# Performance work log

Hardware: AMD Instinct MI355X
Metric: run time of the kernel (lower is better)

## Reference

```python
import jax, jax.numpy as jnp
import numpy as np

N = 128          # cube side (voxels)
LPIX = 3.0       # Mpc per voxel (hardcoded in dsq_loss.forward)
KBINS = 100      # radial k bins (hardcoded)
LOSS_WEIGHT = 1.0


def _binning(n, lpix, kbins):
    # Static radial k-bin assignment computed once with numpy.
    kf = 2.0 * np.pi * np.fft.fftfreq(n, d=lpix)
    kx, ky, kz = np.meshgrid(kf, kf, kf, indexing='ij')
    kmag = np.sqrt(kx * kx + ky * ky + kz * kz).ravel()  # [n^3]
    pos = kmag > 0
    edges = np.linspace(kmag[pos].min(), kmag.max(), kbins + 1)
    ids = np.clip(np.digitize(kmag, edges) - 1, 0, kbins - 1)
    ids = np.where(pos, ids, kbins)  # route k=0 (DC) mode to a dropped bin
    counts = np.bincount(ids[pos], minlength=kbins).astype(np.float32)
    kcent = 0.5 * (edges[:-1] + edges[1:])
    return ids.astype(np.int32), counts, kcent.astype(np.float32)

_IDS, _COUNTS, _KCENT = _binning(N, LPIX, KBINS)


def _dsq(x):
    # x: [B, 1, N, N, N] -> dimensionless power spectrum Delta^2(k): [B, KBINS]
    b = x.shape[0]
    fk = jnp.fft.fftn(x, axes=(-3, -2, -1))
    # P(k) estimator: |delta_k|^2 * Lpix^3 / N^3  (Lpix^6/V with V=(N*Lpix)^3)
    pk = (fk.real ** 2 + fk.imag ** 2) * (LPIX ** 3 / float(N ** 3))
    pk = pk.reshape(b, -1).T  # [N^3, B]
    sums = jax.ops.segment_sum(pk, jnp.asarray(_IDS), num_segments=KBINS + 1)[:KBINS]
    cnt = jnp.asarray(_COUNTS)[:, None]
    pmean = jnp.where(cnt > 0, sums / jnp.maximum(cnt, 1.0), jnp.nan)  # [KBINS, B]
    kc = jnp.asarray(_KCENT)[:, None]
    dsq = pmean * kc ** 3 / (2.0 * jnp.pi ** 2)
    return dsq.T  # [B, KBINS]


def setup_inputs() -> dict:
    key = jax.random.key(0)
    k1, k2 = jax.random.split(key)
    # positive brightness-temperature-like fields so log10(Delta^2) is finite
    pred = jax.random.uniform(k1, (8, 1, N, N, N), dtype=jnp.float32) + 0.1
    target = jax.random.uniform(k2, (8, 1, N, N, N), dtype=jnp.float32) + 0.1
    return {"pred": pred, "target": target}


def reference(pred, target):
    dsq_hr = _dsq(target)
    dsq_sr = _dsq(pred)
    loss = jnp.nanmean(jnp.abs(jnp.log10(dsq_hr) - jnp.log10(dsq_sr)))
    return LOSS_WEIGHT * loss
```

## Files before the change

kernel.cpp:

```cpp
#include <hip/hip_runtime.h>
#include <math.h>

#ifndef M_PI
#define M_PI 3.14159265358979323846
#endif

#define NSIDE 128
#define NVOX  2097152
#define KBINS 100
#define NFIELDS 16
#define NORMF (27.0f / 2097152.0f)
#define FSTRIDE ((size_t)65 * 16384)


#define WS_SUMS_OFF   0
#define WS_CNT_OFF    6464
#define WS_OCT_OFF    8192
#define WS_TRANS_OFF  282880

__device__ __forceinline__ double bin_edge(int i, double start, double step, double stop) {
    if (i == 100) return stop;
    return __dadd_rn(__dmul_rn((double)i, step), start);
}

__device__ __forceinline__ void bin_params(double* start, double* step, double* stop) {
    const double inv   = 1.0 / 384.0;
    const double twopi = 2.0 * M_PI;
    double k1 = __dmul_rn(twopi, __dmul_rn(1.0, inv));
    *start = sqrt(__dadd_rn(__dadd_rn(0.0, 0.0), __dmul_rn(k1, k1)));
    double k64 = __dmul_rn(twopi, __dmul_rn(-64.0, inv));
    double s64 = __dmul_rn(k64, k64);
    *stop = sqrt(__dadd_rn(__dadd_rn(s64, s64), s64));
    *step = (*stop - *start) / 100.0;
}

__device__ int compute_bin(int ix, int iy, int iz) {
    const double inv   = 1.0 / 384.0;
    const double twopi = 2.0 * M_PI;
    double fx = (double)(ix < 64 ? ix : ix - 128);
    double fy = (double)(iy < 64 ? iy : iy - 128);
    double fz = (double)(iz < 64 ? iz : iz - 128);
    double kx = __dmul_rn(twopi, __dmul_rn(fx, inv));
    double ky = __dmul_rn(twopi, __dmul_rn(fy, inv));
    double kz = __dmul_rn(twopi, __dmul_rn(fz, inv));
    double sq = __dadd_rn(__dadd_rn(__dmul_rn(kx, kx), __dmul_rn(ky, ky)), __dmul_rn(kz, kz));
    double kmag = sqrt(sq);
    if (!(kmag > 0.0)) return 100;
    double start, step, stop;
    bin_params(&start, &step, &stop);
    double t = (kmag - start) / step;
    int c = (int)floor(t);
    if (c < -1) c = -1;
    if (c > 100) c = 100;
    while (c < 100 && kmag >= bin_edge(c + 1, start, step, stop)) ++c;
    while (c >= 0 && kmag < bin_edge(c, start, step, stop)) --c;
    if (c < 0) c = 0;
    if (c > 99) c = 99;
    return c;
}

__device__ __forceinline__ int br3(int v) { return ((v & 1) << 2) | (v & 2) | ((v >> 2) & 1); }
__device__ __forceinline__ int br4(int v) {
    return ((v & 1) << 3) | ((v & 2) << 1) | ((v & 4) >> 1) | ((v & 8) >> 3);
}

__device__ __forceinline__ float2 f2add(float2 a, float2 b) { return make_float2(a.x + b.x, a.y + b.y); }
__device__ __forceinline__ float2 f2sub(float2 a, float2 b) { return make_float2(a.x - b.x, a.y - b.y); }
__device__ __forceinline__ float2 cmul(float2 a, float2 w) {
    return make_float2(a.x * w.x - a.y * w.y, a.x * w.y + a.y * w.x);
}
__device__ __forceinline__ float2 twid(float r) {
    return make_float2(__builtin_amdgcn_cosf(r), __builtin_amdgcn_sinf(r));
}

__device__ __forceinline__ void fft128_r16(float2 r[16], int m) {
    const float fm = (float)m;
#pragma unroll
    for (int j = 0; j < 8; ++j) {
        float2 W = twid(-(fm + 8.0f * (float)j) * (1.0f / 128.0f));
        float2 a = r[j], b = r[j + 8];
        r[j]     = f2add(a, b);
        r[j + 8] = cmul(f2sub(a, b), W);
    }
#pragma unroll
    for (int j = 0; j < 4; ++j) {
        float2 W = twid(-(fm + 8.0f * (float)j) * (1.0f / 64.0f));
#pragma unroll
        for (int half = 0; half < 16; half += 8) {
            float2 a = r[half + j], b = r[half + j + 4];
            r[half + j]     = f2add(a, b);
            r[half + j + 4] = cmul(f2sub(a, b), W);
        }
    }
#pragma unroll
    for (int j = 0; j < 2; ++j) {
        float2 W = twid(-(fm + 8.0f * (float)j) * (1.0f / 32.0f));
#pragma unroll
        for (int q = 0; q < 16; q += 4) {
            float2 a = r[q + j], b = r[q + j + 2];
            r[q + j]     = f2add(a, b);
            r[q + j + 2] = cmul(f2sub(a, b), W);
        }
    }
    {
        float2 W = twid(-fm * (1.0f / 16.0f));
#pragma unroll
        for (int q = 0; q < 16; q += 2) {
            float2 a = r[q], b = r[q + 1];
            r[q]     = f2add(a, b);
            r[q + 1] = cmul(f2sub(a, b), W);
        }
    }
#pragma unroll
    for (int h = 4; h >= 2; h >>= 1) {
        bool hi = (m & h) != 0;
        float2 W = twid(-(float)(m & (h - 1)) / (float)(2 * h));
#pragma unroll
        for (int j = 0; j < 16; ++j) {
            float2 x = r[j];
            float2 v = make_float2(__shfl_xor(x.x, h, 64), __shfl_xor(x.y, h, 64));
            float2 s = f2add(x, v);
            float2 d = cmul(f2sub(v, x), W);
            r[j] = hi ? d : s;
        }
    }
    {
        bool hi = (m & 1) != 0;
#pragma unroll
        for (int j = 0; j < 16; ++j) {
            float2 x = r[j];
            float2 v = make_float2(__shfl_xor(x.x, 1, 64), __shfl_xor(x.y, 1, 64));
            r[j] = hi ? f2sub(v, x) : f2add(x, v);
        }
    }
}

__device__ __forceinline__ void fft128_c16(float2 r[16], int m) {
    const float S2 = 0.70710678118654752f;
    {
        int q = m & 3;
        float2 Wm = make_float2(q == 0 ? 1.f : (q == 1 ? S2 : (q == 2 ? 0.f : -S2)),
                                q == 0 ? 0.f : (q == 2 ? -1.f : -S2));
        bool hi = (m & 4) != 0;
        const float2 C[16] = {
            {1.f,0.f},{0.99879546f,-0.04906767f},{0.99518473f,-0.09801714f},
            {0.98917651f,-0.14673047f},{0.98078528f,-0.19509032f},{0.97003125f,-0.24298018f},
            {0.95694034f,-0.29028468f},{0.94154407f,-0.33688985f},{0.92387953f,-0.38268343f},
            {0.90398929f,-0.42755509f},{0.88192126f,-0.47139674f},{0.85772861f,-0.51410274f},
            {0.83146961f,-0.55557023f},{0.80320753f,-0.59569930f},{0.77301045f,-0.63439328f},
            {0.74095113f,-0.67155895f} };
#pragma unroll
        for (int j = 0; j < 16; ++j) {
            float2 x = r[j];
            float2 v = make_float2(__shfl_xor(x.x, 4, 64), __shfl_xor(x.y, 4, 64));
            float2 s = f2add(x, v);
            float2 d = cmul(cmul(f2sub(v, x), Wm), C[j]);
            r[j] = hi ? d : s;
        }
    }
    {
        bool w = (m & 1) != 0;
        bool hi = (m & 2) != 0;
        const float2 C[16] = {
            {1.f,0.f},{0.99518473f,-0.09801714f},{0.98078528f,-0.19509032f},
            {0.95694034f,-0.29028468f},{0.92387953f,-0.38268343f},{0.88192126f,-0.47139674f},
            {0.83146961f,-0.55557023f},{0.77301045f,-0.63439328f},{S2,-S2},
            {0.63439328f,-0.77301045f},{0.55557023f,-0.83146961f},{0.47139674f,-0.88192126f},
            {0.38268343f,-0.92387953f},{0.29028468f,-0.95694034f},{0.19509032f,-0.98078528f},
            {0.09801714f,-0.99518473f} };
#pragma unroll
        for (int j = 0; j < 16; ++j) {
            float2 x = r[j];
            float2 v = make_float2(__shfl_xor(x.x, 2, 64), __shfl_xor(x.y, 2, 64));
            float2 s = f2add(x, v);
            float2 d = f2sub(v, x);
            d = w ? make_float2(d.y, -d.x) : d;
            d = cmul(d, C[j]);
            r[j] = hi ? d : s;
        }
    }
    {
        bool hi = (m & 1) != 0;
        const float2 C[16] = {
            {1.f,0.f},{0.98078528f,-0.19509032f},{0.92387953f,-0.38268343f},
            {0.83146961f,-0.55557023f},{S2,-S2},{0.55557023f,-0.83146961f},
            {0.38268343f,-0.92387953f},{0.19509032f,-0.98078528f},{0.f,-1.f},
            {-0.19509032f,-0.98078528f},{-0.38268343f,-0.92387953f},{-0.55557023f,-0.83146961f},
            {-S2,-S2},{-0.83146961f,-0.55557023f},{-0.92387953f,-0.38268343f},
            {-0.98078528f,-0.19509032f} };
#pragma unroll
        for (int j = 0; j < 16; ++j) {
            float2 x = r[j];
            float2 v = make_float2(__shfl_xor(x.x, 1, 64), __shfl_xor(x.y, 1, 64));
            float2 s = f2add(x, v);
            float2 d = cmul(f2sub(v, x), C[j]);
            r[j] = hi ? d : s;
        }
    }
    {
        const float2 C[8] = {
            {1.f,0.f},{0.92387953f,-0.38268343f},{S2,-S2},{0.38268343f,-0.92387953f},
            {0.f,-1.f},{-0.38268343f,-0.92387953f},{-S2,-S2},{-0.92387953f,-0.38268343f} };
#pragma unroll
        for (int j = 0; j < 8; ++j) {
            float2 a = r[j], b = r[j + 8];
            r[j]     = f2add(a, b);
            r[j + 8] = cmul(f2sub(a, b), C[j]);
        }
    }
    {
        const float2 C[4] = { {1.f,0.f},{S2,-S2},{0.f,-1.f},{-S2,-S2} };
#pragma unroll
        for (int q = 0; q < 16; q += 8)
#pragma unroll
            for (int j = 0; j < 4; ++j) {
                float2 a = r[q + j], b = r[q + j + 4];
                r[q + j]     = f2add(a, b);
                r[q + j + 4] = cmul(f2sub(a, b), C[j]);
            }
    }
    {
#pragma unroll
        for (int q = 0; q < 16; q += 4) {
            { float2 a = r[q], b = r[q + 2]; r[q] = f2add(a, b); r[q + 2] = f2sub(a, b); }
            { float2 a = r[q + 1], b = r[q + 3]; float2 d = f2sub(a, b);
              r[q + 1] = f2add(a, b); r[q + 3] = make_float2(d.y, -d.x); }
        }
    }
    {
#pragma unroll
        for (int q = 0; q < 16; q += 2) {
            float2 a = r[q], b = r[q + 1];
            r[q] = f2add(a, b); r[q + 1] = f2sub(a, b);
        }
    }
}

__global__ __launch_bounds__(256) void k_zero(float* sums, int* counts) {
    int t = blockIdx.x * 256 + threadIdx.x;
    if (t < NFIELDS * 101) sums[t] = 0.0f;
    if (t < 101) counts[t] = 0;
}

__global__ __launch_bounds__(256) void k_oct(unsigned char* __restrict__ oct,
                                             int* __restrict__ counts) {
    __shared__ int lcnt[4][104];
    int tid = threadIdx.x;
#pragma unroll
    for (int j = tid; j < 4 * 104; j += 256) ((int*)lcnt)[j] = 0;
    __syncthreads();
    int idx = blockIdx.x * 256 + tid;
    if (idx < 65 * 65 * 65) {
        int c = idx % 65;
        int r = idx / 65;
        int b = r % 65;
        int a = r / 65;
        int id = compute_bin(a, b, c);
        oct[c * 4225 + a * 65 + b] = (unsigned char)id;
        if (id < 100) {
            int w = ((a == 0 || a == 64) ? 1 : 2) *
                    ((b == 0 || b == 64) ? 1 : 2) *
                    ((c == 0 || c == 64) ? 1 : 2);
            atomicAdd(&lcnt[tid & 3][id], w);
        }
    }
    __syncthreads();
    if (tid < 101) {
        int tot = lcnt[0][tid] + lcnt[1][tid] + lcnt[2][tid] + lcnt[3][tid];
        if (tot) atomicAdd(&counts[tid], tot);
    }
}

__global__ __launch_bounds__(512, 4) void k_fft_zy(const float* __restrict__ pred,
                                                   const float* __restrict__ target,
                                                   float2* __restrict__ A) {
    __shared__ float2 lds[65][132];
    int t = threadIdx.x;
    int m = t & 7, row = t >> 3;
    int x = blockIdx.x;
    int f = blockIdx.y;
    const float* in = (f < 8) ? (pred + (size_t)f * NVOX)
                              : (target + (size_t)(f - 8) * NVOX);

    int b3 = br3(m);
#pragma unroll
    for (int y0 = 0; y0 < 128; y0 += 64) {
        int y = y0 + row;
        const float4* s4 = reinterpret_cast<const float4*>(
            in + (size_t)x * 16384 + (size_t)y * 128 + 16 * m);
        float2 r[16];
#pragma unroll
        for (int q = 0; q < 4; ++q) {
            float4 v = s4[q];
            r[4 * q + 0] = make_float2(v.x, 0.f);
            r[4 * q + 1] = make_float2(v.y, 0.f);
            r[4 * q + 2] = make_float2(v.z, 0.f);
            r[4 * q + 3] = make_float2(v.w, 0.f);
        }
        fft128_c16(r, m);
#pragma unroll
        for (int j = 0; j < 16; j += 2) {
            int kz = 8 * br4(j) + b3;
            lds[kz][y] = r[j];
        }
        if (m == 0) lds[64][y] = r[1];
    }
    __syncthreads();

    float2* basef = A + (size_t)f * FSTRIDE + (size_t)x * 8;
#pragma unroll
    for (int k0 = 0; k0 < 128; k0 += 64) {
        int kz = k0 + row;
        if (kz <= 64) {
            float2 r[16];
#pragma unroll
            for (int j = 0; j < 16; ++j) r[j] = lds[kz][m + 8 * j];
            fft128_r16(r, m);
            float2* dst = basef + (size_t)kz * 16384;
#pragma unroll
            for (int j = 0; j < 16; ++j) dst[j * 1024 + m] = r[j];
        }
    }
}

__global__ __launch_bounds__(256, 6) void k_fft_x_bin(const float2* __restrict__ A,
                                                      const unsigned char* __restrict__ oct,
                                                      float* __restrict__ sums) {
    __shared__ __align__(16) float lbins[8][104];
    __shared__ __align__(16) unsigned char ltab[4384];
    int t = threadIdx.x;
    int m = t & 7, g = t >> 3;
    int kz = blockIdx.x >> 2;
    int s0 = (blockIdx.x & 3) << 5;
    int f = blockIdx.y;
    int p = s0 + g;

    const float2* base = A + (size_t)f * FSTRIDE + (size_t)kz * 16384
                           + (size_t)(p >> 3) * 1024 + (p & 7);
    float2 r[16];
#pragma unroll
    for (int j = 0; j < 16; ++j) r[j] = base[8 * m + 64 * j];

    if (t < 208) ((float4*)lbins)[t] = make_float4(0.f, 0.f, 0.f, 0.f);
    int rowb = kz * 4225;
    int ab   = rowb & ~15;
    int pad  = rowb & 15;
    const uint4* osrc = (const uint4*)(oct + ab);
    ((uint4*)ltab)[t] = osrc[t];
    if (t < 14) ((uint4*)ltab)[256 + t] = osrc[256 + t];

    asm volatile("" : "+v"(r[0]), "+v"(r[1]), "+v"(r[2]), "+v"(r[3]),
                      "+v"(r[4]), "+v"(r[5]), "+v"(r[6]), "+v"(r[7]),
                      "+v"(r[8]), "+v"(r[9]), "+v"(r[10]), "+v"(r[11]),
                      "+v"(r[12]), "+v"(r[13]), "+v"(r[14]), "+v"(r[15]));
    fft128_r16(r, m);
    __syncthreads();

    const unsigned char* lt = ltab + pad;
    int ky = (br3(p & 7) << 4) | br4(p >> 3);
    int mky = (ky <= 64) ? ky : 128 - ky;
    int b3x = br3(m) << 4;
#pragma unroll
    for (int j = 0; j < 16; ++j) {
        int kx = b3x | br4(j);
        int mkx = (kx <= 64) ? kx : 128 - kx;
        float pk = r[j].x * r[j].x + r[j].y * r[j].y;
        atomicAdd(&lbins[t & 7][lt[mkx * 65 + mky]], pk);
    }
    __syncthreads();
    if (t < 101) {
        float wz = (kz == 0 || kz == 64) ? 1.0f : 2.0f;
        float v = lbins[0][t] + lbins[1][t] + lbins[2][t] + lbins[3][t] +
                  lbins[4][t] + lbins[5][t] + lbins[6][t] + lbins[7][t];
        if (v != 0.0f) atomicAdd(&sums[f * 101 + t], v * (NORMF) * wz);
    }
}

__global__ __launch_bounds__(128) void k_finalize(const float* __restrict__ sums,
                                                  const int* __restrict__ counts,
                                                  float* __restrict__ out) {
    __shared__ double ssum[128];
    __shared__ int scnt[128];
    int k = threadIdx.x;
    double local = 0.0;
    int nloc = 0;
    if (k < KBINS) {
        int c = counts[k];
        if (c > 0) {
            double start, step, stop;
            bin_params(&start, &step, &stop);
            double e0 = bin_edge(k, start, step, stop);
            double e1 = bin_edge(k + 1, start, step, stop);
            float kc  = (float)(0.5 * (e0 + e1));
            float kc3 = kc * kc * kc;
            const float two_pi2 = (float)(2.0 * M_PI * M_PI);
            float cf = (float)c;
            for (int b = 0; b < 8; ++b) {
                float pm_p = sums[b * 101 + k] / cf;
                float pm_t = sums[(8 + b) * 101 + k] / cf;
                float dsq_p = pm_p * kc3 / two_pi2;
                float dsq_t = pm_t * kc3 / two_pi2;
                float d = fabsf(log10f(dsq_t) - log10f(dsq_p));
                local += (double)d;
            }
            nloc = 8;
        }
    }
    ssum[k] = local;
    scnt[k] = nloc;
    __syncthreads();
    for (int off = 64; off > 0; off >>= 1) {
        if (k < off) { ssum[k] += ssum[k + off]; scnt[k] += scnt[k + off]; }
        __syncthreads();
    }
    if (k == 0) out[0] = (float)(ssum[0] / (double)scnt[0]);
}

extern "C" void kernel_launch(void* const* d_in, const int* in_sizes, int n_in,
                              void* d_out, int out_size, void* d_ws, size_t ws_size,
                              hipStream_t stream) {
    (void)in_sizes; (void)n_in; (void)out_size; (void)ws_size;
    const float* pred   = (const float*)d_in[0];
    const float* target = (const float*)d_in[1];
    float* out = (float*)d_out;
    char* ws = (char*)d_ws;

    float* sums        = (float*)(ws + WS_SUMS_OFF);
    int* counts        = (int*)(ws + WS_CNT_OFF);
    unsigned char* oct = (unsigned char*)(ws + WS_OCT_OFF);
    float2* A          = (float2*)(ws + WS_TRANS_OFF);

    k_zero<<<7, 256, 0, stream>>>(sums, counts);
    k_oct<<<(65 * 65 * 65 + 255) / 256, 256, 0, stream>>>(oct, counts);

    k_fft_zy<<<dim3(128, NFIELDS), 512, 0, stream>>>(pred, target, A);
    k_fft_x_bin<<<dim3(65 * 4, NFIELDS), 256, 0, stream>>>(A, oct, sums);

    k_finalize<<<1, 128, 0, stream>>>(sums, counts, out);
}
```

Measured before the change: 322.0 us.

## Fuse finalize into x-FFT binning kernel and run-length merge bin atomics

Removes the separate finalize launch: the last block of the x-FFT/binning kernel, found with a global atomic counter, computes the loss. Bin lookups now read the octant table straight from global memory instead of staging it in LDS. Consecutive modes that fall in the same bin are accumulated in registers before one LDS atomic, which cuts atomic traffic. The z-y kernel's kz loop is restructured so only row 0 handles the Nyquist plane, and occupancy hints change from 6 to 4 blocks, which adds tail-block serialisation and extra global byte loads in exchange.

```diff
diff --git a/kernel.cpp b/kernel.cpp
--- a/kernel.cpp
+++ b/kernel.cpp
@@ -11,10 +11,12 @@
 #define NFIELDS 16
 #define NORMF (27.0f / 2097152.0f)
 #define FSTRIDE ((size_t)65 * 16384)
+#define NBLK_XBIN (65 * 4 * NFIELDS)
 
 
 #define WS_SUMS_OFF   0
 #define WS_CNT_OFF    6464
+#define WS_CTR_OFF    7936
 #define WS_OCT_OFF    8192
 #define WS_TRANS_OFF  282880
 
@@ -236,10 +238,11 @@
     }
 }
 
-__global__ __launch_bounds__(256) void k_zero(float* sums, int* counts) {
+__global__ __launch_bounds__(256) void k_zero(float* sums, int* counts, int* ctr) {
     int t = blockIdx.x * 256 + threadIdx.x;
     if (t < NFIELDS * 101) sums[t] = 0.0f;
     if (t < 101) counts[t] = 0;
+    if (t == 101) *ctr = 0;
 }
 
 __global__ __launch_bounds__(256) void k_oct(unsigned char* __restrict__ oct,
@@ -308,26 +311,37 @@
     __syncthreads();
 
     float2* basef = A + (size_t)f * FSTRIDE + (size_t)x * 8;
-#pragma unroll
-    for (int k0 = 0; k0 < 128; k0 += 64) {
-        int kz = k0 + row;
-        if (kz <= 64) {
-            float2 r[16];
-#pragma unroll
-            for (int j = 0; j < 16; ++j) r[j] = lds[kz][m + 8 * j];
-            fft128_r16(r, m);
-            float2* dst = basef + (size_t)kz * 16384;
-#pragma unroll
-            for (int j = 0; j < 16; ++j) dst[j * 1024 + m] = r[j];
-        }
-    }
-}
-
-__global__ __launch_bounds__(256, 6) void k_fft_x_bin(const float2* __restrict__ A,
+    {
+        int kz = row;
+        float2 r[16];
+#pragma unroll
+        for (int j = 0; j < 16; ++j) r[j] = lds[kz][m + 8 * j];
+        fft128_r16(r, m);
+        float2* dst = basef + (size_t)kz * 16384;
+#pragma unroll
+        for (int j = 0; j < 16; ++j) dst[j * 1024 + m] = r[j];
+    }
+    if (row == 0) {
+        float2 r[16];
+#pragma unroll
+        for (int j = 0; j < 16; ++j) r[j] = lds[64][m + 8 * j];
+        fft128_r16(r, m);
+        float2* dst = basef + (size_t)64 * 16384;
+#pragma unroll
+        for (int j = 0; j < 16; ++j) dst[j * 1024 + m] = r[j];
+    }
+}
+
+__global__ __launch_bounds__(256, 4) void k_fft_x_bin(const float2* __restrict__ A,
                                                       const unsigned char* __restrict__ oct,
-                                                      float* __restrict__ sums) {
+                                                      float* __restrict__ sums,
+                                                      const int* __restrict__ counts,
+                                                      int* __restrict__ ctr,
+                                                      float* __restrict__ out) {
     __shared__ __align__(16) float lbins[8][104];
-    __shared__ __align__(16) unsigned char ltab[4384];
+    __shared__ double ssum[256];
+    __shared__ int scnt[256];
+    __shared__ int lastFlag;
     int t = threadIdx.x;
     int m = t & 7, g = t >> 3;
     int kz = blockIdx.x >> 2;
@@ -335,69 +349,80 @@
     int f = blockIdx.y;
     int p = s0 + g;
 
+    if (t < 208) ((float4*)lbins)[t] = make_float4(0.f, 0.f, 0.f, 0.f);
+    __syncthreads();
+
     const float2* base = A + (size_t)f * FSTRIDE + (size_t)kz * 16384
                            + (size_t)(p >> 3) * 1024 + (p & 7);
     float2 r[16];
 #pragma unroll
     for (int j = 0; j < 16; ++j) r[j] = base[8 * m + 64 * j];
-
-    if (t < 208) ((float4*)lbins)[t] = make_float4(0.f, 0.f, 0.f, 0.f);
-    int rowb = kz * 4225;
-    int ab   = rowb & ~15;
-    int pad  = rowb & 15;
-    const uint4* osrc = (const uint4*)(oct + ab);
-    ((uint4*)ltab)[t] = osrc[t];
-    if (t < 14) ((uint4*)ltab)[256 + t] = osrc[256 + t];
-
-    asm volatile("" : "+v"(r[0]), "+v"(r[1]), "+v"(r[2]), "+v"(r[3]),
-                      "+v"(r[4]), "+v"(r[5]), "+v"(r[6]), "+v"(r[7]),
-                      "+v"(r[8]), "+v"(r[9]), "+v"(r[10]), "+v"(r[11]),
-                      "+v"(r[12]), "+v"(r[13]), "+v"(r[14]), "+v"(r[15]));
     fft128_r16(r, m);
-    __syncthreads();
-
-    const unsigned char* lt = ltab + pad;
+
     int ky = (br3(p & 7) << 4) | br4(p >> 3);
     int mky = (ky <= 64) ? ky : 128 - ky;
     int b3x = br3(m) << 4;
-#pragma unroll
-    for (int j = 0; j < 16; ++j) {
-        int kx = b3x | br4(j);
+    const unsigned char* lt = oct + kz * 4225;
+    int bs[16];
+#pragma unroll
+    for (int jj = 0; jj < 16; ++jj) {
+        int kx = b3x + jj;
         int mkx = (kx <= 64) ? kx : 128 - kx;
-        float pk = r[j].x * r[j].x + r[j].y * r[j].y;
-        atomicAdd(&lbins[t & 7][lt[mkx * 65 + mky]], pk);
-    }
-    __syncthreads();
+        bs[jj] = lt[mkx * 65 + mky];
+    }
+
+    {
+        float2 v0 = r[br4(0)];
+        float acc = v0.x * v0.x + v0.y * v0.y;
+        int cur = bs[0];
+#pragma unroll
+        for (int jj = 1; jj < 16; ++jj) {
+            float2 v = r[br4(jj)];
+            float pk = v.x * v.x + v.y * v.y;
+            if (bs[jj] == cur) {
+                acc += pk;
+            } else {
+                atomicAdd(&lbins[m][cur], acc);
+                cur = bs[jj];
+                acc = pk;
+            }
+        }
+        atomicAdd(&lbins[m][cur], acc);
+    }
+    __syncthreads();
+
     if (t < 101) {
         float wz = (kz == 0 || kz == 64) ? 1.0f : 2.0f;
         float v = lbins[0][t] + lbins[1][t] + lbins[2][t] + lbins[3][t] +
                   lbins[4][t] + lbins[5][t] + lbins[6][t] + lbins[7][t];
         if (v != 0.0f) atomicAdd(&sums[f * 101 + t], v * (NORMF) * wz);
     }
-}
-
-__global__ __launch_bounds__(128) void k_finalize(const float* __restrict__ sums,
-                                                  const int* __restrict__ counts,
-                                                  float* __restrict__ out) {
-    __shared__ double ssum[128];
-    __shared__ int scnt[128];
-    int k = threadIdx.x;
+
+    __threadfence();
+    if (t == 0) lastFlag = (atomicAdd(ctr, 1) == NBLK_XBIN - 1);
+    __syncthreads();
+    if (!lastFlag) return;
+
     double local = 0.0;
     int nloc = 0;
-    if (k < KBINS) {
-        int c = counts[k];
+    if (t < KBINS) {
+        int c = __hip_atomic_load(&counts[t], __ATOMIC_RELAXED, __HIP_MEMORY_SCOPE_AGENT);
         if (c > 0) {
             double start, step, stop;
             bin_params(&start, &step, &stop);
-            double e0 = bin_edge(k, start, step, stop);
-            double e1 = bin_edge(k + 1, start, step, stop);
+            double e0 = bin_edge(t, start, step, stop);
+            double e1 = bin_edge(t + 1, start, step, stop);
             float kc  = (float)(0.5 * (e0 + e1));
             float kc3 = kc * kc * kc;
             const float two_pi2 = (float)(2.0 * M_PI * M_PI);
             float cf = (float)c;
             for (int b = 0; b < 8; ++b) {
-                float pm_p = sums[b * 101 + k] / cf;
-                float pm_t = sums[(8 + b) * 101 + k] / cf;
+                float sp = __hip_atomic_load(&sums[b * 101 + t], __ATOMIC_RELAXED,
+                                             __HIP_MEMORY_SCOPE_AGENT);
+                float st = __hip_atomic_load(&sums[(8 + b) * 101 + t], __ATOMIC_RELAXED,
+                                             __HIP_MEMORY_SCOPE_AGENT);
+            float pm_p = sp / cf;
+                float pm_t = st / cf;
                 float dsq_p = pm_p * kc3 / two_pi2;
                 float dsq_t = pm_t * kc3 / two_pi2;
                 float d = fabsf(log10f(dsq_t) - log10f(dsq_p));
@@ -406,14 +431,14 @@
             nloc = 8;
         }
     }
-    ssum[k] = local;
-    scnt[k] = nloc;
-    __syncthreads();
-    for (int off = 64; off > 0; off >>= 1) {
-        if (k < off) { ssum[k] += ssum[k + off]; scnt[k] += scnt[k + off]; }
+    ssum[t] = local;
+    scnt[t] = nloc;
+    __syncthreads();
+    for (int off = 128; off > 0; off >>= 1) {
+        if (t < off) { ssum[t] += ssum[t + off]; scnt[t] += scnt[t + off]; }
         __syncthreads();
     }
-    if (k == 0) out[0] = (float)(ssum[0] / (double)scnt[0]);
+    if (t == 0) out[0] = (float)(ssum[0] / (double)scnt[0]);
 }
 
 extern "C" void kernel_launch(void* const* d_in, const int* in_sizes, int n_in,
@@ -427,14 +452,13 @@
 
     float* sums        = (float*)(ws + WS_SUMS_OFF);
     int* counts        = (int*)(ws + WS_CNT_OFF);
+    int* ctr           = (int*)(ws + WS_CTR_OFF);
     unsigned char* oct = (unsigned char*)(ws + WS_OCT_OFF);
     float2* A          = (float2*)(ws + WS_TRANS_OFF);
 
-    k_zero<<<7, 256, 0, stream>>>(sums, counts);
+    k_zero<<<7, 256, 0, stream>>>(sums, counts, ctr);
     k_oct<<<(65 * 65 * 65 + 255) / 256, 256, 0, stream>>>(oct, counts);
 
     k_fft_zy<<<dim3(128, NFIELDS), 512, 0, stream>>>(pred, target, A);
-    k_fft_x_bin<<<dim3(65 * 4, NFIELDS), 256, 0, stream>>>(A, oct, sums);
-
-    k_finalize<<<1, 128, 0, stream>>>(sums, counts, out);
-}
+    k_fft_x_bin<<<dim3(65 * 4, NFIELDS), 256, 0, stream>>>(A, oct, sums, counts, ctr, out);
+}
```

Result: slower. 579.6 us (+80.0%).

## Fuse octant table build into FFT kernel and finalize via last-block pattern

Applied to the files above, without the earlier changes.

Cuts five launches down to a memset plus two kernels. The octant bin table and mode counts are now computed by an extra row of blocks in the z/y FFT kernel, reusing its shared memory. The final log-ratio reduction runs inside the x-FFT/binning kernel, done by whichever block is last to increment a global atomic counter. This removes launch and inter-kernel gaps, in exchange for a threadfence and an atomic per block, plus added shared memory in the binning kernel that may lower occupancy.

```diff
diff --git a/kernel.cpp b/kernel.cpp
--- a/kernel.cpp
+++ b/kernel.cpp
@@ -11,10 +11,12 @@
 #define NFIELDS 16
 #define NORMF (27.0f / 2097152.0f)
 #define FSTRIDE ((size_t)65 * 16384)
+#define NBLK_XBIN (65 * 4 * NFIELDS)
 
 
 #define WS_SUMS_OFF   0
 #define WS_CNT_OFF    6464
+#define WS_CTR_OFF    7936
 #define WS_OCT_OFF    8192
 #define WS_TRANS_OFF  282880
 
@@ -236,49 +238,43 @@
     }
 }
 
-__global__ __launch_bounds__(256) void k_zero(float* sums, int* counts) {
-    int t = blockIdx.x * 256 + threadIdx.x;
-    if (t < NFIELDS * 101) sums[t] = 0.0f;
-    if (t < 101) counts[t] = 0;
-}
-
-__global__ __launch_bounds__(256) void k_oct(unsigned char* __restrict__ oct,
-                                             int* __restrict__ counts) {
-    __shared__ int lcnt[4][104];
-    int tid = threadIdx.x;
-#pragma unroll
-    for (int j = tid; j < 4 * 104; j += 256) ((int*)lcnt)[j] = 0;
-    __syncthreads();
-    int idx = blockIdx.x * 256 + tid;
-    if (idx < 65 * 65 * 65) {
-        int c = idx % 65;
-        int r = idx / 65;
-        int b = r % 65;
-        int a = r / 65;
-        int id = compute_bin(a, b, c);
-        oct[c * 4225 + a * 65 + b] = (unsigned char)id;
-        if (id < 100) {
-            int w = ((a == 0 || a == 64) ? 1 : 2) *
-                    ((b == 0 || b == 64) ? 1 : 2) *
-                    ((c == 0 || c == 64) ? 1 : 2);
-            atomicAdd(&lcnt[tid & 3][id], w);
-        }
-    }
-    __syncthreads();
-    if (tid < 101) {
-        int tot = lcnt[0][tid] + lcnt[1][tid] + lcnt[2][tid] + lcnt[3][tid];
-        if (tot) atomicAdd(&counts[tid], tot);
-    }
-}
-
-__global__ __launch_bounds__(512, 4) void k_fft_zy(const float* __restrict__ pred,
+__global__ __launch_bounds__(512, 4) void k_zy_oct(const float* __restrict__ pred,
                                                    const float* __restrict__ target,
-                                                   float2* __restrict__ A) {
+                                                   float2* __restrict__ A,
+                                                   unsigned char* __restrict__ oct,
+                                                   int* __restrict__ counts) {
     __shared__ float2 lds[65][132];
     int t = threadIdx.x;
+
+    if (blockIdx.y == 0) {
+        int* lcnt = (int*)&lds[0][0];
+        for (int j = t; j < 4 * 104; j += 512) lcnt[j] = 0;
+        __syncthreads();
+        for (int idx = blockIdx.x * 512 + t; idx < 65 * 65 * 65; idx += 128 * 512) {
+            int c = idx % 65;
+            int r = idx / 65;
+            int b = r % 65;
+            int a = r / 65;
+            int id = compute_bin(a, b, c);
+            oct[c * 4225 + a * 65 + b] = (unsigned char)id;
+            if (id < 100) {
+                int w = ((a == 0 || a == 64) ? 1 : 2) *
+                        ((b == 0 || b == 64) ? 1 : 2) *
+                        ((c == 0 || c == 64) ? 1 : 2);
+                atomicAdd(&lcnt[(t & 3) * 104 + id], w);
+            }
+        }
+        __syncthreads();
+        if (t < 101) {
+            int tot = lcnt[t] + lcnt[104 + t] + lcnt[208 + t] + lcnt[312 + t];
+            if (tot) atomicAdd(&counts[t], tot);
+        }
+        return;
+    }
+
     int m = t & 7, row = t >> 3;
     int x = blockIdx.x;
-    int f = blockIdx.y;
+    int f = blockIdx.y - 1;
     const float* in = (f < 8) ? (pred + (size_t)f * NVOX)
                               : (target + (size_t)(f - 8) * NVOX);
 
@@ -325,9 +321,15 @@
 
 __global__ __launch_bounds__(256, 6) void k_fft_x_bin(const float2* __restrict__ A,
                                                       const unsigned char* __restrict__ oct,
-                                                      float* __restrict__ sums) {
+                                                      float* __restrict__ sums,
+                                                      const int* __restrict__ counts,
+                                                      int* __restrict__ ctr,
+                                                      float* __restrict__ out) {
     __shared__ __align__(16) float lbins[8][104];
     __shared__ __align__(16) unsigned char ltab[4384];
+    __shared__ double ssum[256];
+    __shared__ int scnt[256];
+    __shared__ int lastFlag;
     int t = threadIdx.x;
     int m = t & 7, g = t >> 3;
     int kz = blockIdx.x >> 2;
@@ -374,30 +376,32 @@
                   lbins[4][t] + lbins[5][t] + lbins[6][t] + lbins[7][t];
         if (v != 0.0f) atomicAdd(&sums[f * 101 + t], v * (NORMF) * wz);
     }
-}
-
-__global__ __launch_bounds__(128) void k_finalize(const float* __restrict__ sums,
-                                                  const int* __restrict__ counts,
-                                                  float* __restrict__ out) {
-    __shared__ double ssum[128];
-    __shared__ int scnt[128];
-    int k = threadIdx.x;
+
+    __threadfence();
+    if (t == 0) lastFlag = (atomicAdd(ctr, 1) == NBLK_XBIN - 1);
+    __syncthreads();
+    if (!lastFlag) return;
+
     double local = 0.0;
     int nloc = 0;
-    if (k < KBINS) {
-        int c = counts[k];
+    if (t < KBINS) {
+        int c = __hip_atomic_load(&counts[t], __ATOMIC_RELAXED, __HIP_MEMORY_SCOPE_AGENT);
         if (c > 0) {
             double start, step, stop;
             bin_params(&start, &step, &stop);
-            double e0 = bin_edge(k, start, step, stop);
-            double e1 = bin_edge(k + 1, start, step, stop);
+            double e0 = bin_edge(t, start, step, stop);
+            double e1 = bin_edge(t + 1, start, step, stop);
             float kc  = (float)(0.5 * (e0 + e1));
             float kc3 = kc * kc * kc;
             const float two_pi2 = (float)(2.0 * M_PI * M_PI);
             float cf = (float)c;
             for (int b = 0; b < 8; ++b) {
-                float pm_p = sums[b * 101 + k] / cf;
-                float pm_t = sums[(8 + b) * 101 + k] / cf;
+                float sp = __hip_atomic_load(&sums[b * 101 + t], __ATOMIC_RELAXED,
+                                             __HIP_MEMORY_SCOPE_AGENT);
+                float st = __hip_atomic_load(&sums[(8 + b) * 101 + t], __ATOMIC_RELAXED,
+                                             __HIP_MEMORY_SCOPE_AGENT);
+                float pm_p = sp / cf;
+                float pm_t = st / cf;
                 float dsq_p = pm_p * kc3 / two_pi2;
                 float dsq_t = pm_t * kc3 / two_pi2;
                 float d = fabsf(log10f(dsq_t) - log10f(dsq_p));
@@ -406,14 +410,14 @@
             nloc = 8;
         }
     }
-    ssum[k] = local;
-    scnt[k] = nloc;
+    ssum[t] = local;
+    scnt[t] = nloc;
     __syncthreads();
-    for (int off = 64; off > 0; off >>= 1) {
-        if (k < off) { ssum[k] += ssum[k + off]; scnt[k] += scnt[k + off]; }
+    for (int off = 128; off > 0; off >>= 1) {
+        if (t < off) { ssum[t] += ssum[t + off]; scnt[t] += scnt[t + off]; }
         __syncthreads();
     }
-    if (k == 0) out[0] = (float)(ssum[0] / (double)scnt[0]);
+    if (t == 0) out[0] = (float)(ssum[0] / (double)scnt[0]);
 }
 
 extern "C" void kernel_launch(void* const* d_in, const int* in_sizes, int n_in,
@@ -427,14 +431,12 @@
 
     float* sums        = (float*)(ws + WS_SUMS_OFF);
     int* counts        = (int*)(ws + WS_CNT_OFF);
+    int* ctr           = (int*)(ws + WS_CTR_OFF);
     unsigned char* oct = (unsigned char*)(ws + WS_OCT_OFF);
     float2* A          = (float2*)(ws + WS_TRANS_OFF);
 
-    k_zero<<<7, 256, 0, stream>>>(sums, counts);
-    k_oct<<<(65 * 65 * 65 + 255) / 256, 256, 0, stream>>>(oct, counts);
-
-    k_fft_zy<<<dim3(128, NFIELDS), 512, 0, stream>>>(pred, target, A);
-    k_fft_x_bin<<<dim3(65 * 4, NFIELDS), 256, 0, stream>>>(A, oct, sums);
-
-    k_finalize<<<1, 128, 0, stream>>>(sums, counts, out);
-}
+    hipMemsetAsync(ws, 0, 8192, stream);
+
+    k_zy_oct<<<dim3(128, NFIELDS + 1), 512, 0, stream>>>(pred, target, A, oct, counts);
+    k_fft_x_bin<<<dim3(65 * 4, NFIELDS), 256, 0, stream>>>(A, oct, sums, counts, ctr, out);
+}
```

Measured after the change: 512.0 us. 59.0% more time.
